# Kernel optimization log

Measured on AMD Instinct MI355X. Metric: run time of the kernel, lower is better.

Reference implementation:

```python
import math
import jax, jax.numpy as jnp
import numpy as np

V = 32000   # vocab_size
NL = 8      # n_layer
NH = 16     # n_head
D = 1024    # n_embd
DH = D // NH
FF = 4 * D
B = 2
L = 1024
EPS = 1e-5


def setup_inputs() -> dict:
    key = jax.random.key(0)
    ks = jax.random.split(key, 10)
    std = 0.02  # matches nn.init.normal_(std=0.02)
    def nrm(k, shape):
        return jax.random.normal(k, shape, jnp.float32) * std
    return {
        "idx": jax.random.randint(ks[0], (B, L), 0, V),
        "tok_emb": nrm(ks[1], (V, D)),
        # per-layer params stacked on leading NL axis (scanned over)
        "ln1_w": jnp.ones((NL, D)), "ln1_b": jnp.zeros((NL, D)),
        "wq": nrm(ks[2], (NL, D, D)), "wk": nrm(ks[3], (NL, D, D)),
        "wv": nrm(ks[4], (NL, D, D)), "wo": nrm(ks[5], (NL, D, D)),
        "ln2_w": jnp.ones((NL, D)), "ln2_b": jnp.zeros((NL, D)),
        "w1": nrm(ks[6], (NL, D, FF)), "b1": jnp.zeros((NL, FF)),
        "w2": nrm(ks[7], (NL, FF, D)), "b2": jnp.zeros((NL, D)),
        "lnf_w": jnp.ones((D,)), "lnf_b": jnp.zeros((D,)),
        "lm_head": nrm(ks[8], (D, V)),
    }


def _sinusoidal_pe(seq_len, dim):
    pos = jnp.arange(seq_len, dtype=jnp.float32)[:, None]
    div = jnp.exp(jnp.arange(0, dim, 2, dtype=jnp.float32) * (-math.log(10000.0) / dim))
    pe = jnp.zeros((seq_len, dim), jnp.float32)
    pe = pe.at[:, 0::2].set(jnp.sin(pos * div))
    pe = pe.at[:, 1::2].set(jnp.cos(pos * div))
    return pe


def _ln(x, w, b):
    m = x.mean(-1, keepdims=True)
    v = ((x - m) ** 2).mean(-1, keepdims=True)
    return (x - m) * jax.lax.rsqrt(v + EPS) * w + b


def reference(idx, tok_emb, ln1_w, ln1_b, wq, wk, wv, wo,
              ln2_w, ln2_b, w1, b1, w2, b2, lnf_w, lnf_b, lm_head):
    b, l = idx.shape
    x = tok_emb[idx] + _sinusoidal_pe(l, tok_emb.shape[1])[None]  # [B,L,D]
    causal = jnp.tril(jnp.ones((l, l), bool))
    scale = 1.0 / math.sqrt(DH)

    def block(x, p):
        l1w, l1b, Wq, Wk, Wv, Wo, l2w, l2b, W1, B1, W2, B2 = p
        h = _ln(x, l1w, l1b)
        def heads(W):  # [B,L,D] -> [B,H,L,DH]
            return (h @ W).reshape(b, l, NH, DH).transpose(0, 2, 1, 3)
        q, k, v = heads(Wq), heads(Wk), heads(Wv)
        att = jnp.einsum('bhqd,bhkd->bhqk', q, k) * scale
        att = jnp.where(causal, att, -jnp.inf)
        att = jax.nn.softmax(att, axis=-1)
        y = jnp.einsum('bhqk,bhkd->bhqd', att, v)
        y = y.transpose(0, 2, 1, 3).reshape(b, l, -1)
        x = x + y @ Wo
        h2 = _ln(x, l2w, l2b)
        x = x + jax.nn.gelu(h2 @ W1 + B1, approximate=False) @ W2 + B2
        return x, None

    x, _ = jax.lax.scan(
        block, x, (ln1_w, ln1_b, wq, wk, wv, wo, ln2_w, ln2_b, w1, b1, w2, b2))
    x = _ln(x, lnf_w, lnf_b)
    return x @ lm_head  # [B,L,V] logits
```

## Files before the change

kernel.cpp:

```cpp
#include <hip/hip_runtime.h>
#include <math.h>

typedef unsigned short u16;
typedef __bf16 bfx8 __attribute__((ext_vector_type(8)));
typedef float f32x4 __attribute__((ext_vector_type(4)));

#define NLAYER  8
#define NHEAD   16
#define DMODEL  1024
#define DHEAD   64
#define DFF     4096
#define NB      2
#define SEQ     1024
#define NVOCAB  32000
#define NTOK    (NB*SEQ)
#define EPSLN   1e-5f
#define VCHUNK  6400
#define NSPLIT  2

__device__ __forceinline__ float bf2f(u16 u) {
  union { unsigned int i; float f; } x; x.i = ((unsigned int)u) << 16; return x.f;
}
__device__ __forceinline__ u16 f2bf(float f) {
  unsigned int x = __float_as_uint(f);
  x += 0x7fffu + ((x >> 16) & 1u);
  return (u16)(x >> 16);
}

#if defined(__has_builtin)
#if __has_builtin(__builtin_amdgcn_global_load_lds)
#define HAVE_GLL 1
#endif
#endif

__device__ __forceinline__ void gll16(const void* g, void* lds_base, int lane) {
#ifdef HAVE_GLL
  __builtin_amdgcn_global_load_lds((const __attribute__((address_space(1))) unsigned int*)g,
                                   (__attribute__((address_space(3))) unsigned int*)lds_base,
                                   16, 0, 0);
  (void)lane;
#else
  *(uint4*)((char*)lds_base + lane * 16) = *(const uint4*)g;
#endif
}

enum { EPI_QKV = 0, EPI_GELU_BIAS = 1, EPI_RESID = 2, EPI_RESID_BIAS = 3, EPI_LOGITS = 4 };

template <int EPI, int BM>
__global__ __launch_bounds__(256) void gemm_bt(
    const u16* __restrict__ A, const u16* __restrict__ Bt,
    const float* __restrict__ bias, u16* __restrict__ outb,
    float* __restrict__ outf, int M, int N, int K, int ldc)
{
  constexpr int ARND = BM / 32;
  constexpr int MF = BM / 32;
  __shared__ __align__(16) u16 sA[BM * 64];
  __shared__ __align__(16) u16 sB[128 * 64];

  const int tid  = threadIdx.x;
  const int w    = tid >> 6;
  const int lane = tid & 63;
  const int l16  = lane & 15;
  const int hi   = lane >> 4;
  const int wm   = w >> 1;
  const int wn   = w & 1;

  const int nwg = gridDim.x;
  const int MB  = M / BM;
  const int orig = blockIdx.x;
  const int xcd = orig & 7, li = orig >> 3;
  const int q = nwg >> 3, r = nwg & 7;
  const int work = (xcd < r ? xcd * (q + 1) : r * (q + 1) + (xcd - r) * q) + li;
  const int m0 = (work % MB) * BM;
  const int n0 = (work / MB) * 128;

  const int srow8 = lane >> 3;
  const int su    = lane & 7;

  const u16* gA[ARND]; const u16* gB[4];
  char* lA[ARND]; char* lB[4];
#pragma unroll
  for (int r2 = 0; r2 < ARND; r2++) {
    const int row = r2 * 32 + w * 8 + srow8;
    const int gu = su ^ (row & 7);
    gA[r2] = A + (size_t)(m0 + row) * K + gu * 8;
    lA[r2] = (char*)sA + (r2 * 32 + w * 8) * 128;
  }
#pragma unroll
  for (int r2 = 0; r2 < 4; r2++) {
    const int row = r2 * 32 + w * 8 + srow8;
    const int gu = su ^ (row & 7);
    gB[r2] = Bt + (size_t)(n0 + row) * K + gu * 8;
    lB[r2] = (char*)sB + (r2 * 32 + w * 8) * 128;
  }

  f32x4 acc[MF][4];
#pragma unroll
  for (int i = 0; i < MF; i++)
#pragma unroll
    for (int j = 0; j < 4; j++)
#pragma unroll
      for (int r2 = 0; r2 < 4; r2++) acc[i][j][r2] = 0.0f;

  for (int k0 = 0; k0 < K; k0 += 64) {
#pragma unroll
    for (int r2 = 0; r2 < ARND; r2++) { gll16(gA[r2], lA[r2], lane); gA[r2] += 64; }
#pragma unroll
    for (int r2 = 0; r2 < 4; r2++)    { gll16(gB[r2], lB[r2], lane); gB[r2] += 64; }
    __syncthreads();

    bfx8 aF[MF][2], bF[4][2];
#pragma unroll
    for (int i = 0; i < MF; i++) {
      const int row = wm * (BM / 2) + i * 16 + l16;
      const int rsw = row & 7;
#pragma unroll
      for (int kk = 0; kk < 2; kk++)
        aF[i][kk] = *(const bfx8*)((const char*)sA + row * 128 + ((kk * 4 + hi) ^ rsw) * 16);
    }
#pragma unroll
    for (int j = 0; j < 4; j++) {
      const int row = wn * 64 + j * 16 + l16;
      const int rsw = row & 7;
#pragma unroll
      for (int kk = 0; kk < 2; kk++)
        bF[j][kk] = *(const bfx8*)((const char*)sB + row * 128 + ((kk * 4 + hi) ^ rsw) * 16);
    }
#pragma unroll
    for (int kk = 0; kk < 2; kk++)
#pragma unroll
      for (int i = 0; i < MF; i++)
#pragma unroll
        for (int j = 0; j < 4; j++)
          acc[i][j] = __builtin_amdgcn_mfma_f32_16x16x32_bf16(aF[i][kk], bF[j][kk], acc[i][j], 0, 0, 0);
    __syncthreads();
  }

  const int rbase = m0 + wm * (BM / 2);
  const int cbase = n0 + wn * 64;
#pragma unroll
  for (int i = 0; i < MF; i++) {
#pragma unroll
    for (int j = 0; j < 4; j++) {
      const int gcol = cbase + j * 16 + l16;
      float bv = 0.0f;
      if constexpr (EPI == EPI_GELU_BIAS || EPI == EPI_RESID_BIAS) bv = bias[gcol];
#pragma unroll
      for (int r2 = 0; r2 < 4; r2++) {
        const int grow = rbase + i * 16 + hi * 4 + r2;
        float v = acc[i][j][r2];
        const size_t oi = (size_t)grow * ldc + gcol;
        if constexpr (EPI == EPI_QKV) {
          outb[oi] = f2bf(v);
        } else if constexpr (EPI == EPI_GELU_BIAS) {
          v += bv;
          v = 0.5f * v * (1.0f + erff(v * 0.70710678118654752f));
          outb[oi] = f2bf(v);
        } else if constexpr (EPI == EPI_RESID) {
          outf[oi] += v;
        } else if constexpr (EPI == EPI_RESID_BIAS) {
          outf[oi] += v + bv;
        } else {
          outf[oi] = v;
        }
      }
    }
  }
}

__global__ __launch_bounds__(256) void ln_kernel(
    const float* __restrict__ x, const float* __restrict__ w,
    const float* __restrict__ b, u16* __restrict__ out)
{
  const int row = blockIdx.x;
  const int tid = threadIdx.x;
  const float* xr = x + (size_t)row * DMODEL;
  float4 v = *(const float4*)(xr + tid * 4);
  __shared__ float sbuf[4];
  float s = v.x + v.y + v.z + v.w;
#pragma unroll
  for (int o = 32; o > 0; o >>= 1) s += __shfl_xor(s, o, 64);
  if ((tid & 63) == 0) sbuf[tid >> 6] = s;
  __syncthreads();
  const float mean = (sbuf[0] + sbuf[1] + sbuf[2] + sbuf[3]) * (1.0f / DMODEL);
  __syncthreads();
  float d0 = v.x - mean, d1 = v.y - mean, d2 = v.z - mean, d3 = v.w - mean;
  float qq = d0 * d0 + d1 * d1 + d2 * d2 + d3 * d3;
#pragma unroll
  for (int o = 32; o > 0; o >>= 1) qq += __shfl_xor(qq, o, 64);
  if ((tid & 63) == 0) sbuf[tid >> 6] = qq;
  __syncthreads();
  const float var = (sbuf[0] + sbuf[1] + sbuf[2] + sbuf[3]) * (1.0f / DMODEL);
  const float rstd = rsqrtf(var + EPSLN);
  const int c = tid * 4;
  float dv[4] = {d0, d1, d2, d3};
#pragma unroll
  for (int e = 0; e < 4; e++)
    out[(size_t)row * DMODEL + c + e] = f2bf(dv[e] * rstd * w[c + e] + b[c + e]);
}

__global__ __launch_bounds__(256) void embed_kernel(
    const int* __restrict__ idx, const float* __restrict__ tok, float* __restrict__ x)
{
  const int row = blockIdx.x;
  const int l = row & (SEQ - 1);
  const int t = idx[row];
  const int d = threadIdx.x * 4;
#pragma unroll
  for (int e = 0; e < 4; e++) {
    const int dd = d + e;
    const float freq = expf((float)(dd & ~1) * (-9.210340371976184f / (float)DMODEL));
    const float ang = (float)l * freq;
    const float pe = (dd & 1) ? cosf(ang) : sinf(ang);
    x[(size_t)row * DMODEL + dd] = tok[(size_t)t * DMODEL + dd] + pe;
  }
}

__global__ __launch_bounds__(256) void transpose_kernel(
    const float* __restrict__ in, u16* __restrict__ out, int rows, int cols)
{
  __shared__ float tile[32][33];
  const int c0 = blockIdx.x * 32, r0 = blockIdx.y * 32;
  const int tx = threadIdx.x & 31, ty = threadIdx.x >> 5;
#pragma unroll
  for (int i = ty; i < 32; i += 8)
    tile[i][tx] = in[(size_t)(r0 + i) * cols + c0 + tx];
  __syncthreads();
#pragma unroll
  for (int i = ty; i < 32; i += 8)
    out[(size_t)(c0 + i) * rows + r0 + tx] = f2bf(tile[tx][i]);
}

__global__ __launch_bounds__(256) void transpose4_kernel(
    const float* __restrict__ i0, const float* __restrict__ i1,
    const float* __restrict__ i2, const float* __restrict__ i3,
    u16* __restrict__ o0, u16* __restrict__ o1,
    u16* __restrict__ o2, u16* __restrict__ o3)
{
  __shared__ float tile[32][33];
  const int z = blockIdx.z;
  const float* in = (z == 0) ? i0 : (z == 1) ? i1 : (z == 2) ? i2 : i3;
  u16* out = (z == 0) ? o0 : (z == 1) ? o1 : (z == 2) ? o2 : o3;
  const int c0 = blockIdx.x * 32, r0 = blockIdx.y * 32;
  const int tx = threadIdx.x & 31, ty = threadIdx.x >> 5;
#pragma unroll
  for (int i = ty; i < 32; i += 8)
    tile[i][tx] = in[(size_t)(r0 + i) * DMODEL + c0 + tx];
  __syncthreads();
#pragma unroll
  for (int i = ty; i < 32; i += 8)
    out[(size_t)(c0 + i) * DMODEL + r0 + tx] = f2bf(tile[tx][i]);
}

__global__ __launch_bounds__(256) void vtrans_kernel(
    const u16* __restrict__ qkv, u16* __restrict__ vt)
{
  __shared__ u16 tile[32][33];
  const int bh = blockIdx.z;
  const int b = bh >> 4, hh = bh & 15;
  const int l0 = blockIdx.x * 32, d0 = blockIdx.y * 32;
  const int tx = threadIdx.x & 31, ty = threadIdx.x >> 5;
#pragma unroll
  for (int i = ty; i < 32; i += 8)
    tile[i][tx] = qkv[(size_t)(b * SEQ + l0 + i) * (3 * DMODEL) + 2 * DMODEL + hh * DHEAD + d0 + tx];
  __syncthreads();
#pragma unroll
  for (int i = ty; i < 32; i += 8)
    vt[(size_t)(bh * DHEAD + d0 + i) * SEQ + l0 + tx] = tile[tx][i];
}

__device__ __forceinline__ int plds_byte(int row, int col) {
  return row * 128 + ((((col >> 3) ^ (row & 7)) << 3) + (col & 7)) * 2;
}

__global__ __launch_bounds__(64) void attn_partial(
    const u16* __restrict__ qkv, const u16* __restrict__ vt,
    float* __restrict__ opart, float* __restrict__ mpart, float* __restrict__ lpart)
{
  __shared__ __align__(16) u16 p_lds[32 * 64];
  const int lane = threadIdx.x;
  const int l16 = lane & 15, hi = lane >> 4;
  const int qt = blockIdx.x, hh = blockIdx.y;
  const int b = blockIdx.z >> 1, sp = blockIdx.z & 1;
  const int q0 = qt * 32;
  const int T = (q0 + 95) >> 6;
  const int t_lo = (T * sp) >> 1;
  const int t_hi = (T * (sp + 1)) >> 1;

  const u16* qptr = qkv;
  const u16* kptr = qkv + DMODEL;
  const size_t rs3 = 3 * DMODEL;
  const size_t hoff = (size_t)hh * DHEAD;

  bfx8 aQ[2][2];
#pragma unroll
  for (int mt = 0; mt < 2; mt++)
#pragma unroll
    for (int kf = 0; kf < 2; kf++)
      aQ[mt][kf] = *(const bfx8*)&qptr[(size_t)(b * SEQ + q0 + mt * 16 + l16) * rs3 + hoff + kf * 32 + hi * 8];

  f32x4 o[2][4];
  float mrun[2][4], ssum[2][4];
#pragma unroll
  for (int mt = 0; mt < 2; mt++)
#pragma unroll
    for (int r = 0; r < 4; r++) { mrun[mt][r] = -__builtin_inff(); ssum[mt][r] = 0.0f; }
#pragma unroll
  for (int mt = 0; mt < 2; mt++)
#pragma unroll
    for (int dt = 0; dt < 4; dt++)
#pragma unroll
      for (int r = 0; r < 4; r++) o[mt][dt][r] = 0.0f;

  for (int kt = t_lo; kt < t_hi; kt++) {
    const int k0 = kt * 64;
    const bool diag = (kt == T - 1);

    bfx8 bK[4][2];
#pragma unroll
    for (int nt = 0; nt < 4; nt++)
#pragma unroll
      for (int kf = 0; kf < 2; kf++)
        bK[nt][kf] = *(const bfx8*)&kptr[(size_t)(b * SEQ + k0 + nt * 16 + l16) * rs3 + hoff + kf * 32 + hi * 8];

    f32x4 s[2][4];
#pragma unroll
    for (int mt = 0; mt < 2; mt++)
#pragma unroll
      for (int nt = 0; nt < 4; nt++) {
#pragma unroll
        for (int r = 0; r < 4; r++) s[mt][nt][r] = 0.0f;
        s[mt][nt] = __builtin_amdgcn_mfma_f32_16x16x32_bf16(aQ[mt][0], bK[nt][0], s[mt][nt], 0, 0, 0);
        s[mt][nt] = __builtin_amdgcn_mfma_f32_16x16x32_bf16(aQ[mt][1], bK[nt][1], s[mt][nt], 0, 0, 0);
      }

#pragma unroll
    for (int mt = 0; mt < 2; mt++) {
#pragma unroll
      for (int r = 0; r < 4; r++) {
        const int row_l = mt * 16 + hi * 4 + r;
        const int qrow = q0 + row_l;
        float sv[4];
#pragma unroll
        for (int nt = 0; nt < 4; nt++) sv[nt] = s[mt][nt][r] * 0.125f;
        if (diag) {
#pragma unroll
          for (int nt = 0; nt < 4; nt++)
            if (k0 + nt * 16 + l16 > qrow) sv[nt] = -__builtin_inff();
        }
        float mx = fmaxf(fmaxf(sv[0], sv[1]), fmaxf(sv[2], sv[3]));
#pragma unroll
        for (int t = 1; t < 16; t <<= 1) mx = fmaxf(mx, __shfl_xor(mx, t, 64));
        const float mnew = fmaxf(mrun[mt][r], mx);
        const float alpha = __expf(mrun[mt][r] - mnew);
        mrun[mt][r] = mnew;
        float p[4], rsum = 0.0f;
#pragma unroll
        for (int nt = 0; nt < 4; nt++) { p[nt] = __expf(sv[nt] - mnew); rsum += p[nt]; }
#pragma unroll
        for (int t = 1; t < 16; t <<= 1) rsum += __shfl_xor(rsum, t, 64);
        ssum[mt][r] = ssum[mt][r] * alpha + rsum;
#pragma unroll
        for (int dt = 0; dt < 4; dt++) o[mt][dt][r] *= alpha;
#pragma unroll
        for (int nt = 0; nt < 4; nt++)
          *(u16*)((char*)p_lds + plds_byte(row_l, nt * 16 + l16)) = f2bf(p[nt]);
      }
    }
    __syncthreads();

    bfx8 pa[2][2];
#pragma unroll
    for (int mt = 0; mt < 2; mt++) {
      const int row = mt * 16 + l16;
#pragma unroll
      for (int kf = 0; kf < 2; kf++)
        pa[mt][kf] = *(const bfx8*)((const char*)p_lds + row * 128 + (((kf * 4 + hi) ^ (row & 7)) << 4));
    }
    bfx8 bV[4][2];
    const size_t vbase = (size_t)(b * NHEAD + hh) * DHEAD * SEQ;
#pragma unroll
    for (int dt = 0; dt < 4; dt++)
#pragma unroll
      for (int kf = 0; kf < 2; kf++)
        bV[dt][kf] = *(const bfx8*)&vt[vbase + (size_t)(dt * 16 + l16) * SEQ + k0 + kf * 32 + hi * 8];
#pragma unroll
    for (int mt = 0; mt < 2; mt++)
#pragma unroll
      for (int dt = 0; dt < 4; dt++) {
        o[mt][dt] = __builtin_amdgcn_mfma_f32_16x16x32_bf16(pa[mt][0], bV[dt][0], o[mt][dt], 0, 0, 0);
        o[mt][dt] = __builtin_amdgcn_mfma_f32_16x16x32_bf16(pa[mt][1], bV[dt][1], o[mt][dt], 0, 0, 0);
      }
    __syncthreads();
  }

  const size_t pbase = (((size_t)sp * NB + b) * NHEAD + hh) * SEQ + q0;
#pragma unroll
  for (int mt = 0; mt < 2; mt++) {
#pragma unroll
    for (int r = 0; r < 4; r++) {
      const int row_l = mt * 16 + hi * 4 + r;
      const size_t rg = pbase + row_l;
      if (l16 == 0) { mpart[rg] = mrun[mt][r]; lpart[rg] = ssum[mt][r]; }
#pragma unroll
      for (int dt = 0; dt < 4; dt++)
        opart[rg * DHEAD + dt * 16 + l16] = o[mt][dt][r];
    }
  }
}

__global__ __launch_bounds__(256) void attn_combine(
    const float* __restrict__ opart, const float* __restrict__ mpart,
    const float* __restrict__ lpart, u16* __restrict__ y)
{
  const int row = blockIdx.x;
  const int b = row >> 10;
  const int l = row & (SEQ - 1);
  const int t = threadIdx.x;
  const int hh = t >> 4;
  const int d0 = (t & 15) * 4;
  const size_t r0 = ((size_t)b * NHEAD + hh) * SEQ + l;
  const size_t r1 = (size_t)NB * NHEAD * SEQ + r0;
  const float m0 = mpart[r0], m1 = mpart[r1];
  const float l0 = lpart[r0], l1 = lpart[r1];
  const float mm = fmaxf(m0, m1);
  const float w0 = __expf(m0 - mm), w1 = __expf(m1 - mm);
  const float dn = 1.0f / (w0 * l0 + w1 * l1);
  const float4 o0 = *(const float4*)&opart[r0 * DHEAD + d0];
  const float4 o1 = *(const float4*)&opart[r1 * DHEAD + d0];
  u16* yp = y + (size_t)row * DMODEL + hh * DHEAD + d0;
  yp[0] = f2bf((w0 * o0.x + w1 * o1.x) * dn);
  yp[1] = f2bf((w0 * o0.y + w1 * o1.y) * dn);
  yp[2] = f2bf((w0 * o0.z + w1 * o1.z) * dn);
  yp[3] = f2bf((w0 * o0.w + w1 * o1.w) * dn);
}

extern "C" void kernel_launch(void* const* d_in, const int* in_sizes, int n_in,
                              void* d_out, int out_size, void* d_ws, size_t ws_size,
                              hipStream_t stream)
{
  (void)in_sizes; (void)n_in; (void)out_size;
  const int*   idx  = (const int*)d_in[0];
  const float* tok  = (const float*)d_in[1];
  const float* ln1w = (const float*)d_in[2];
  const float* ln1b = (const float*)d_in[3];
  const float* wq   = (const float*)d_in[4];
  const float* wk   = (const float*)d_in[5];
  const float* wv   = (const float*)d_in[6];
  const float* wo   = (const float*)d_in[7];
  const float* ln2w = (const float*)d_in[8];
  const float* ln2b = (const float*)d_in[9];
  const float* w1   = (const float*)d_in[10];
  const float* b1   = (const float*)d_in[11];
  const float* w2   = (const float*)d_in[12];
  const float* b2   = (const float*)d_in[13];
  const float* lnfw = (const float*)d_in[14];
  const float* lnfb = (const float*)d_in[15];
  const float* lmh  = (const float*)d_in[16];
  float* out = (float*)d_out;

  char* ws = (char*)d_ws;
  size_t off = 0;
  auto alloc = [&](size_t bytes) -> void* {
    void* p = ws + off;
    off += (bytes + 255) & ~(size_t)255;
    return p;
  };
  float* x  = (float*)alloc((size_t)NTOK * DMODEL * 4);
  u16* h    = (u16*)alloc((size_t)NTOK * DMODEL * 2);
  u16* qkv  = (u16*)alloc((size_t)NTOK * 3 * DMODEL * 2);
  u16* vtb  = (u16*)alloc((size_t)NTOK * DMODEL * 2);
  u16* yb   = (u16*)alloc((size_t)NTOK * DMODEL * 2);
  u16* ffb  = (u16*)alloc((size_t)NTOK * DFF * 2);
  float* opart = (float*)alloc((size_t)NSPLIT * NB * NHEAD * SEQ * DHEAD * 4);
  float* mpart = (float*)alloc((size_t)NSPLIT * NB * NHEAD * SEQ * 4);
  float* lpart = (float*)alloc((size_t)NSPLIT * NB * NHEAD * SEQ * 4);
  u16* wT   = (u16*)alloc((size_t)12 * 1024 * 1024 * 2);

  const size_t lmhT_bytes = (size_t)NVOCAB * DMODEL * 2;
  const bool full_lmh = (off + lmhT_bytes) <= ws_size;
  u16* lmhT = full_lmh ? (u16*)alloc(lmhT_bytes) : nullptr;

  u16* wqT = wT;
  u16* wkT = wT + (size_t)DMODEL * DMODEL;
  u16* wvT = wT + 2 * (size_t)DMODEL * DMODEL;
  u16* woT = wT + 3 * (size_t)DMODEL * DMODEL;
  u16* w1T = wT + 4 * (size_t)DMODEL * DMODEL;
  u16* w2T = w1T + (size_t)DMODEL * DFF;

  embed_kernel<<<NTOK, 256, 0, stream>>>(idx, tok, x);

  const int gQKV = (3 * DMODEL / 128) * (NTOK / 128);
  const int gFF1 = (DFF / 128) * (NTOK / 128);
  const int gD64 = (DMODEL / 128) * (NTOK / 64);

  for (int layer = 0; layer < NLAYER; layer++) {
    const float* lwq = wq + (size_t)layer * DMODEL * DMODEL;
    const float* lwk = wk + (size_t)layer * DMODEL * DMODEL;
    const float* lwv = wv + (size_t)layer * DMODEL * DMODEL;
    const float* lwo = wo + (size_t)layer * DMODEL * DMODEL;
    const float* lw1 = w1 + (size_t)layer * DMODEL * DFF;
    const float* lw2 = w2 + (size_t)layer * DFF * DMODEL;

    transpose4_kernel<<<dim3(DMODEL / 32, DMODEL / 32, 4), 256, 0, stream>>>(
        lwq, lwk, lwv, lwo, wqT, wkT, wvT, woT);
    transpose_kernel<<<dim3(DFF / 32, DMODEL / 32), 256, 0, stream>>>(lw1, w1T, DMODEL, DFF);
    transpose_kernel<<<dim3(DMODEL / 32, DFF / 32), 256, 0, stream>>>(lw2, w2T, DFF, DMODEL);

    ln_kernel<<<NTOK, 256, 0, stream>>>(x, ln1w + layer * DMODEL, ln1b + layer * DMODEL, h);
    gemm_bt<EPI_QKV, 128><<<gQKV, 256, 0, stream>>>(h, wqT, nullptr, qkv, nullptr,
                                                    NTOK, 3 * DMODEL, DMODEL, 3 * DMODEL);
    vtrans_kernel<<<dim3(SEQ / 32, DHEAD / 32, NB * NHEAD), 256, 0, stream>>>(qkv, vtb);
    attn_partial<<<dim3(SEQ / 32, NHEAD, NB * NSPLIT), 64, 0, stream>>>(
        qkv, vtb, opart, mpart, lpart);
    attn_combine<<<NB * SEQ, 256, 0, stream>>>(opart, mpart, lpart, yb);
    gemm_bt<EPI_RESID, 64><<<gD64, 256, 0, stream>>>(yb, woT, nullptr, nullptr, x,
                                                     NTOK, DMODEL, DMODEL, DMODEL);
    ln_kernel<<<NTOK, 256, 0, stream>>>(x, ln2w + layer * DMODEL, ln2b + layer * DMODEL, h);
    gemm_bt<EPI_GELU_BIAS, 128><<<gFF1, 256, 0, stream>>>(h, w1T, b1 + (size_t)layer * DFF, ffb,
                                                          nullptr, NTOK, DFF, DMODEL, DFF);
    gemm_bt<EPI_RESID_BIAS, 64><<<gD64, 256, 0, stream>>>(ffb, w2T, b2 + (size_t)layer * DMODEL,
                                                          nullptr, x, NTOK, DMODEL, DFF, DMODEL);
  }

  ln_kernel<<<NTOK, 256, 0, stream>>>(x, lnfw, lnfb, h);

  if (full_lmh) {
    transpose_kernel<<<dim3(NVOCAB / 32, DMODEL / 32), 256, 0, stream>>>(
        lmh, lmhT, DMODEL, NVOCAB);
    const int gLM = (NVOCAB / 128) * (NTOK / 128);
    gemm_bt<EPI_LOGITS, 128><<<gLM, 256, 0, stream>>>(
        h, lmhT, nullptr, nullptr, out, NTOK, NVOCAB, DMODEL, NVOCAB);
  } else {
    for (int c = 0; c < NVOCAB / VCHUNK; c++) {
      transpose_kernel<<<dim3(VCHUNK / 32, DMODEL / 32), 256, 0, stream>>>(
          lmh + (size_t)c * VCHUNK, wT, DMODEL, NVOCAB);
      gemm_bt<EPI_LOGITS, 128><<<(VCHUNK / 128) * (NTOK / 128), 256, 0, stream>>>(
          h, wT, nullptr, nullptr, out + (size_t)c * VCHUNK,
          NTOK, VCHUNK, DMODEL, NVOCAB);
    }
  }
}
```

Before: 2.135 ms.

## Batch all-layer weight transposes upfront, split attention 4 ways, add MFMA priority

Weight transposes for all layers now run as six batched launches before the layer loop whenever the workspace is large enough, replacing three small launches per layer. The attention KV split grows from 2 to 4, with a generalized combine kernel, to give the causal attention grid more blocks. s_setprio is raised around the MFMA sections so those waves are favoured by the scheduler. The cost is more workspace for the transposed weights of every layer and more partial-result traffic through the combine step.

```diff
diff --git a/kernel.cpp b/kernel.cpp
--- a/kernel.cpp
+++ b/kernel.cpp
@@ -16,7 +16,7 @@
 #define NTOK    (NB*SEQ)
 #define EPSLN   1e-5f
 #define VCHUNK  6400
-#define NSPLIT  2
+#define NSPLIT  4
 
 __device__ __forceinline__ float bf2f(u16 u) {
   union { unsigned int i; float f; } x; x.i = ((unsigned int)u) << 16; return x.f;
@@ -216,10 +216,13 @@
   }
 }
 
-__global__ __launch_bounds__(256) void transpose_kernel(
-    const float* __restrict__ in, u16* __restrict__ out, int rows, int cols)
+__global__ __launch_bounds__(256) void transpose_b(
+    const float* __restrict__ in0, u16* __restrict__ out0, int rows, int cols,
+    size_t in_ls, size_t out_ls)
 {
   __shared__ float tile[32][33];
+  const float* in = in0 + (size_t)blockIdx.z * in_ls;
+  u16* out = out0 + (size_t)blockIdx.z * out_ls;
   const int c0 = blockIdx.x * 32, r0 = blockIdx.y * 32;
   const int tx = threadIdx.x & 31, ty = threadIdx.x >> 5;
 #pragma unroll
@@ -229,27 +232,6 @@
 #pragma unroll
   for (int i = ty; i < 32; i += 8)
     out[(size_t)(c0 + i) * rows + r0 + tx] = f2bf(tile[tx][i]);
-}
-
-__global__ __launch_bounds__(256) void transpose4_kernel(
-    const float* __restrict__ i0, const float* __restrict__ i1,
-    const float* __restrict__ i2, const float* __restrict__ i3,
-    u16* __restrict__ o0, u16* __restrict__ o1,
-    u16* __restrict__ o2, u16* __restrict__ o3)
-{
-  __shared__ float tile[32][33];
-  const int z = blockIdx.z;
-  const float* in = (z == 0) ? i0 : (z == 1) ? i1 : (z == 2) ? i2 : i3;
-  u16* out = (z == 0) ? o0 : (z == 1) ? o1 : (z == 2) ? o2 : o3;
-  const int c0 = blockIdx.x * 32, r0 = blockIdx.y * 32;
-  const int tx = threadIdx.x & 31, ty = threadIdx.x >> 5;
-#pragma unroll
-  for (int i = ty; i < 32; i += 8)
-    tile[i][tx] = in[(size_t)(r0 + i) * DMODEL + c0 + tx];
-  __syncthreads();
-#pragma unroll
-  for (int i = ty; i < 32; i += 8)
-    out[(size_t)(c0 + i) * DMODEL + r0 + tx] = f2bf(tile[tx][i]);
 }
 
 __global__ __launch_bounds__(256) void vtrans_kernel(
@@ -281,11 +263,11 @@
   const int lane = threadIdx.x;
   const int l16 = lane & 15, hi = lane >> 4;
   const int qt = blockIdx.x, hh = blockIdx.y;
-  const int b = blockIdx.z >> 1, sp = blockIdx.z & 1;
+  const int b = blockIdx.z >> 2, sp = blockIdx.z & 3;
   const int q0 = qt * 32;
   const int T = (q0 + 95) >> 6;
-  const int t_lo = (T * sp) >> 1;
-  const int t_hi = (T * (sp + 1)) >> 1;
+  const int t_lo = (T * sp) >> 2;
+  const int t_hi = (T * (sp + 1)) >> 2;
 
   const u16* qptr = qkv;
   const u16* kptr = qkv + DMODEL;
@@ -324,6 +306,7 @@
         bK[nt][kf] = *(const bfx8*)&kptr[(size_t)(b * SEQ + k0 + nt * 16 + l16) * rs3 + hoff + kf * 32 + hi * 8];
 
     f32x4 s[2][4];
+    __builtin_amdgcn_s_setprio(1);
 #pragma unroll
     for (int mt = 0; mt < 2; mt++)
 #pragma unroll
@@ -333,6 +316,7 @@
         s[mt][nt] = __builtin_amdgcn_mfma_f32_16x16x32_bf16(aQ[mt][0], bK[nt][0], s[mt][nt], 0, 0, 0);
         s[mt][nt] = __builtin_amdgcn_mfma_f32_16x16x32_bf16(aQ[mt][1], bK[nt][1], s[mt][nt], 0, 0, 0);
       }
+    __builtin_amdgcn_s_setprio(0);
 
 #pragma unroll
     for (int mt = 0; mt < 2; mt++) {
@@ -384,6 +368,7 @@
 #pragma unroll
       for (int kf = 0; kf < 2; kf++)
         bV[dt][kf] = *(const bfx8*)&vt[vbase + (size_t)(dt * 16 + l16) * SEQ + k0 + kf * 32 + hi * 8];
+    __builtin_amdgcn_s_setprio(1);
 #pragma unroll
     for (int mt = 0; mt < 2; mt++)
 #pragma unroll
@@ -391,6 +376,7 @@
         o[mt][dt] = __builtin_amdgcn_mfma_f32_16x16x32_bf16(pa[mt][0], bV[dt][0], o[mt][dt], 0, 0, 0);
         o[mt][dt] = __builtin_amdgcn_mfma_f32_16x16x32_bf16(pa[mt][1], bV[dt][1], o[mt][dt], 0, 0, 0);
       }
+    __builtin_amdgcn_s_setprio(0);
     __syncthreads();
   }
 
@@ -419,20 +405,32 @@
   const int t = threadIdx.x;
   const int hh = t >> 4;
   const int d0 = (t & 15) * 4;
-  const size_t r0 = ((size_t)b * NHEAD + hh) * SEQ + l;
-  const size_t r1 = (size_t)NB * NHEAD * SEQ + r0;
-  const float m0 = mpart[r0], m1 = mpart[r1];
-  const float l0 = lpart[r0], l1 = lpart[r1];
-  const float mm = fmaxf(m0, m1);
-  const float w0 = __expf(m0 - mm), w1 = __expf(m1 - mm);
-  const float dn = 1.0f / (w0 * l0 + w1 * l1);
-  const float4 o0 = *(const float4*)&opart[r0 * DHEAD + d0];
-  const float4 o1 = *(const float4*)&opart[r1 * DHEAD + d0];
+  const size_t base = ((size_t)b * NHEAD + hh) * SEQ + l;
+  const size_t stride = (size_t)NB * NHEAD * SEQ;
+  float m[NSPLIT], lv[NSPLIT];
+  float mm = -__builtin_inff();
+#pragma unroll
+  for (int i = 0; i < NSPLIT; i++) {
+    m[i] = mpart[base + i * stride];
+    lv[i] = lpart[base + i * stride];
+    mm = fmaxf(mm, m[i]);
+  }
+  float wsum = 0.0f, wv[NSPLIT];
+#pragma unroll
+  for (int i = 0; i < NSPLIT; i++) { wv[i] = __expf(m[i] - mm); wsum += wv[i] * lv[i]; }
+  const float dn = 1.0f / wsum;
+  float4 acc = make_float4(0.f, 0.f, 0.f, 0.f);
+#pragma unroll
+  for (int i = 0; i < NSPLIT; i++) {
+    const float4 ov = *(const float4*)&opart[(base + i * stride) * DHEAD + d0];
+    acc.x += wv[i] * ov.x; acc.y += wv[i] * ov.y;
+    acc.z += wv[i] * ov.z; acc.w += wv[i] * ov.w;
+  }
   u16* yp = y + (size_t)row * DMODEL + hh * DHEAD + d0;
-  yp[0] = f2bf((w0 * o0.x + w1 * o1.x) * dn);
-  yp[1] = f2bf((w0 * o0.y + w1 * o1.y) * dn);
-  yp[2] = f2bf((w0 * o0.z + w1 * o1.z) * dn);
-  yp[3] = f2bf((w0 * o0.w + w1 * o1.w) * dn);
+  yp[0] = f2bf(acc.x * dn);
+  yp[1] = f2bf(acc.y * dn);
+  yp[2] = f2bf(acc.z * dn);
+  yp[3] = f2bf(acc.w * dn);
 }
 
 extern "C" void kernel_launch(void* const* d_in, const int* in_sizes, int n_in,
@@ -475,37 +473,61 @@
   float* opart = (float*)alloc((size_t)NSPLIT * NB * NHEAD * SEQ * DHEAD * 4);
   float* mpart = (float*)alloc((size_t)NSPLIT * NB * NHEAD * SEQ * 4);
   float* lpart = (float*)alloc((size_t)NSPLIT * NB * NHEAD * SEQ * 4);
-  u16* wT   = (u16*)alloc((size_t)12 * 1024 * 1024 * 2);
-
+
+  const size_t perLayerElems = 4 * (size_t)DMODEL * DMODEL + 2 * (size_t)DMODEL * DFF;
+  const size_t wAll_bytes = (size_t)NLAYER * perLayerElems * 2;
+  const size_t wT_bytes = perLayerElems * 2;
   const size_t lmhT_bytes = (size_t)NVOCAB * DMODEL * 2;
-  const bool full_lmh = (off + lmhT_bytes) <= ws_size;
-  u16* lmhT = full_lmh ? (u16*)alloc(lmhT_bytes) : nullptr;
-
-  u16* wqT = wT;
-  u16* wkT = wT + (size_t)DMODEL * DMODEL;
-  u16* wvT = wT + 2 * (size_t)DMODEL * DMODEL;
-  u16* woT = wT + 3 * (size_t)DMODEL * DMODEL;
-  u16* w1T = wT + 4 * (size_t)DMODEL * DMODEL;
-  u16* w2T = w1T + (size_t)DMODEL * DFF;
+
+  int tier;
+  u16 *wAll = nullptr, *wT = nullptr, *lmhT = nullptr;
+  if (off + wAll_bytes + lmhT_bytes <= ws_size) {
+    tier = 2;
+    wAll = (u16*)alloc(wAll_bytes);
+    lmhT = (u16*)alloc(lmhT_bytes);
+  } else if (off + wT_bytes + lmhT_bytes <= ws_size) {
+    tier = 1;
+    wT = (u16*)alloc(wT_bytes);
+    lmhT = (u16*)alloc(lmhT_bytes);
+  } else {
+    tier = 0;
+    wT = (u16*)alloc(wT_bytes);
+  }
 
   embed_kernel<<<NTOK, 256, 0, stream>>>(idx, tok, x);
+
+  if (tier == 2) {
+    const size_t ols = perLayerElems;
+    const size_t dd = (size_t)DMODEL * DMODEL, dff = (size_t)DMODEL * DFF;
+    transpose_b<<<dim3(DMODEL/32, DMODEL/32, NLAYER), 256, 0, stream>>>(wq, wAll,                 DMODEL, DMODEL, dd, ols);
+    transpose_b<<<dim3(DMODEL/32, DMODEL/32, NLAYER), 256, 0, stream>>>(wk, wAll + dd,            DMODEL, DMODEL, dd, ols);
+    transpose_b<<<dim3(DMODEL/32, DMODEL/32, NLAYER), 256, 0, stream>>>(wv, wAll + 2*dd,          DMODEL, DMODEL, dd, ols);
+    transpose_b<<<dim3(DMODEL/32, DMODEL/32, NLAYER), 256, 0, stream>>>(wo, wAll + 3*dd,          DMODEL, DMODEL, dd, ols);
+    transpose_b<<<dim3(DFF/32, DMODEL/32, NLAYER), 256, 0, stream>>>(w1, wAll + 4*dd,             DMODEL, DFF,    dff, ols);
+    transpose_b<<<dim3(DMODEL/32, DFF/32, NLAYER), 256, 0, stream>>>(w2, wAll + 4*dd + dff,       DFF,    DMODEL, dff, ols);
+  }
 
   const int gQKV = (3 * DMODEL / 128) * (NTOK / 128);
   const int gFF1 = (DFF / 128) * (NTOK / 128);
   const int gD64 = (DMODEL / 128) * (NTOK / 64);
 
   for (int layer = 0; layer < NLAYER; layer++) {
-    const float* lwq = wq + (size_t)layer * DMODEL * DMODEL;
-    const float* lwk = wk + (size_t)layer * DMODEL * DMODEL;
-    const float* lwv = wv + (size_t)layer * DMODEL * DMODEL;
-    const float* lwo = wo + (size_t)layer * DMODEL * DMODEL;
-    const float* lw1 = w1 + (size_t)layer * DMODEL * DFF;
-    const float* lw2 = w2 + (size_t)layer * DFF * DMODEL;
-
-    transpose4_kernel<<<dim3(DMODEL / 32, DMODEL / 32, 4), 256, 0, stream>>>(
-        lwq, lwk, lwv, lwo, wqT, wkT, wvT, woT);
-    transpose_kernel<<<dim3(DFF / 32, DMODEL / 32), 256, 0, stream>>>(lw1, w1T, DMODEL, DFF);
-    transpose_kernel<<<dim3(DMODEL / 32, DFF / 32), 256, 0, stream>>>(lw2, w2T, DFF, DMODEL);
+    const size_t dd = (size_t)DMODEL * DMODEL, dff = (size_t)DMODEL * DFF;
+    u16 *wqT, *wkT, *wvT, *woT, *w1T, *w2T;
+    if (tier == 2) {
+      u16* base = wAll + (size_t)layer * perLayerElems;
+      wqT = base; wkT = base + dd; wvT = base + 2*dd; woT = base + 3*dd;
+      w1T = base + 4*dd; w2T = base + 4*dd + dff;
+    } else {
+      wqT = wT; wkT = wT + dd; wvT = wT + 2*dd; woT = wT + 3*dd;
+      w1T = wT + 4*dd; w2T = wT + 4*dd + dff;
+      transpose_b<<<dim3(DMODEL/32, DMODEL/32, 1), 256, 0, stream>>>(wq + layer*dd, wqT, DMODEL, DMODEL, 0, 0);
+      transpose_b<<<dim3(DMODEL/32, DMODEL/32, 1), 256, 0, stream>>>(wk + layer*dd, wkT, DMODEL, DMODEL, 0, 0);
+      transpose_b<<<dim3(DMODEL/32, DMODEL/32, 1), 256, 0, stream>>>(wv + layer*dd, wvT, DMODEL, DMODEL, 0, 0);
+      transpose_b<<<dim3(DMODEL/32, DMODEL/32, 1), 256, 0, stream>>>(wo + layer*dd, woT, DMODEL, DMODEL, 0, 0);
+      transpose_b<<<dim3(DFF/32, DMODEL/32, 1), 256, 0, stream>>>(w1 + layer*dff, w1T, DMODEL, DFF, 0, 0);
+      transpose_b<<<dim3(DMODEL/32, DFF/32, 1), 256, 0, stream>>>(w2 + layer*dff, w2T, DFF, DMODEL, 0, 0);
+    }
 
     ln_kernel<<<NTOK, 256, 0, stream>>>(x, ln1w + layer * DMODEL, ln1b + layer * DMODEL, h);
     gemm_bt<EPI_QKV, 128><<<gQKV, 256, 0, stream>>>(h, wqT, nullptr, qkv, nullptr,
@@ -525,16 +547,15 @@
 
   ln_kernel<<<NTOK, 256, 0, stream>>>(x, lnfw, lnfb, h);
 
-  if (full_lmh) {
-    transpose_kernel<<<dim3(NVOCAB / 32, DMODEL / 32), 256, 0, stream>>>(
-        lmh, lmhT, DMODEL, NVOCAB);
+  if (tier >= 1) {
+    transpose_b<<<dim3(NVOCAB/32, DMODEL/32, 1), 256, 0, stream>>>(lmh, lmhT, DMODEL, NVOCAB, 0, 0);
     const int gLM = (NVOCAB / 128) * (NTOK / 128);
     gemm_bt<EPI_LOGITS, 128><<<gLM, 256, 0, stream>>>(
         h, lmhT, nullptr, nullptr, out, NTOK, NVOCAB, DMODEL, NVOCAB);
   } else {
     for (int c = 0; c < NVOCAB / VCHUNK; c++) {
-      transpose_kernel<<<dim3(VCHUNK / 32, DMODEL / 32), 256, 0, stream>>>(
-          lmh + (size_t)c * VCHUNK, wT, DMODEL, NVOCAB);
+      transpose_b<<<dim3(VCHUNK/32, DMODEL/32, 1), 256, 0, stream>>>(
+          lmh + (size_t)c * VCHUNK, wT, DMODEL, NVOCAB, 0, 0);
       gemm_bt<EPI_LOGITS, 128><<<(VCHUNK / 128) * (NTOK / 128), 256, 0, stream>>>(
           h, wT, nullptr, nullptr, out + (size_t)c * VCHUNK,
           NTOK, VCHUNK, DMODEL, NVOCAB);
```

Result: slower. 2.309 ms (+8.2%).
